# Kernel optimization log

Hardware: AMD Instinct MI355X
Metric: run time of the kernel (lower is better)

The kernel has to match this reference:

```python
import jax, jax.numpy as jnp
import numpy as np

N = 100_000      # num nodes
E = 1_600_000    # num edges
F_IN = 128       # input feature dim
H = 128          # hidden dim
C = 16           # num classes
R = 5            # num relations


def setup_inputs() -> dict:
    key = jax.random.key(0)
    ks = jax.random.split(key, 12)
    x = jax.random.normal(ks[0], (N, F_IN), jnp.float32)
    edge_index = jax.random.randint(ks[1], (2, E), 0, N, dtype=jnp.int64)
    edge_weight = jax.random.uniform(ks[2], (E,), jnp.float32)
    edge_type = jax.random.randint(ks[3], (E,), 0, R, dtype=jnp.int64)
    # RGCNConv params (no basis decomposition): per-relation weight, root, bias
    s1 = 1.0 / np.sqrt(F_IN).astype(np.float32)
    s2 = 1.0 / np.sqrt(H).astype(np.float32)
    W1 = jax.random.normal(ks[4], (R, F_IN, H), jnp.float32) * s1
    root1 = jax.random.normal(ks[5], (F_IN, H), jnp.float32) * s1
    b1 = jnp.zeros((H,), jnp.float32)
    W2 = jax.random.normal(ks[6], (R, H, C), jnp.float32) * s2
    root2 = jax.random.normal(ks[7], (H, C), jnp.float32) * s2
    b2 = jnp.zeros((C,), jnp.float32)
    return {"x": x, "edge_index": edge_index, "edge_weight": edge_weight,
            "edge_type": edge_type, "W1": W1, "root1": root1, "b1": b1,
            "W2": W2, "root2": root2, "b2": b2}


def _rgcn_conv(x, src, dst, ew, et, W, root, b):
    """WeightedRGCNConv: per-relation weighted mean aggregation + relation matmul.

    Equivalent to the torch loop over relations: mask edges of type r,
    propagate with aggr='mean' (PyG RGCNConv default) on messages
    edge_weight * x[src], then h_r @ W[r], summed over r; plus root & bias.
    Vectorized by scattering into (dst, relation) buckets.
    """
    n, r = x.shape[0], W.shape[0]
    m = x[src] * ew[:, None]                       # [E, d_in] messages
    seg = dst * r + et                             # bucket = (dst node, relation)
    sums = jax.ops.segment_sum(m, seg, num_segments=n * r).reshape(n, r, -1)
    cnt = jax.ops.segment_sum(jnp.ones_like(ew), seg, num_segments=n * r)
    cnt = cnt.reshape(n, r, 1)
    agg = sums / jnp.maximum(cnt, 1.0)             # mean; 0 for empty buckets
    out = jnp.einsum('nri,rio->no', agg, W)        # sum_r H_r @ W_r
    return out + x @ root + b


def reference(x, edge_index, edge_weight, edge_type, W1, root1, b1, W2, root2, b2):
    src, dst = edge_index[0], edge_index[1]
    h = _rgcn_conv(x, src, dst, edge_weight, edge_type, W1, root1, b1)
    h = jax.nn.relu(h)  # dropout is identity in eval mode
    out = _rgcn_conv(h, src, dst, edge_weight, edge_type, W2, root2, b2)
    return jax.nn.log_softmax(out, axis=1)
```

## Files before the change

### kernel.cpp

```cpp
#include <hip/hip_runtime.h>

#define N_NODES 100000
#define N_EDGES 1600000
#define N_REL   5
#define M_BUCKETS (N_NODES * N_REL)
#define NCOARSE  196
#define CAP      16384

using bf16x8 = __attribute__((ext_vector_type(8))) short;
using f32x4  = __attribute__((ext_vector_type(4))) float;
using f32x2  = __attribute__((ext_vector_type(2))) float;

__device__ __forceinline__ unsigned short f2bf(float f) {
    unsigned int u = __float_as_uint(f);
    u += 0x7fffu + ((u >> 16) & 1u);
    return (unsigned short)(u >> 16);
}
__device__ __forceinline__ float bflo(unsigned int p) { return __uint_as_float(p << 16); }
__device__ __forceinline__ float bfhi(unsigned int p) { return __uint_as_float(p & 0xffff0000u); }
__device__ __forceinline__ float bfu(unsigned short u) { return __uint_as_float((unsigned int)u << 16); }

__global__ __launch_bounds__(1024) void partition_append(
    const int* __restrict__ src, const int* __restrict__ dstv,
    const float* __restrict__ ew, const int* __restrict__ et,
    int* __restrict__ ccur, int2* __restrict__ pe) {
    __shared__ int lh[256];
    __shared__ int lb[256];
    int tid = threadIdx.x;
    if (tid < 256) lh[tid] = 0;
    __syncthreads();
    int base = blockIdx.x * 4096;
    int key[4], rank[4], meta[4];
    float w[4];
    #pragma unroll
    for (int i = 0; i < 4; ++i) {
        int e = base + i * 1024 + tid;
        key[i] = -1;
        if (e < N_EDGES) {
            int d = dstv[e];
            key[i] = d >> 9;
            meta[i] = src[e] | (et[e] << 17) | ((d & 511) << 20);
            w[i] = ew[e];
            rank[i] = atomicAdd(&lh[key[i]], 1);
        }
    }
    __syncthreads();
    if (tid < 256) {
        int c = lh[tid];
        lb[tid] = c ? atomicAdd(&ccur[tid], c) : 0;
    }
    __syncthreads();
    #pragma unroll
    for (int i = 0; i < 4; ++i)
        if (key[i] >= 0) {
            int pos = lb[key[i]] + rank[i];
            if (pos < CAP)
                pe[((size_t)key[i] << 14) + pos] = make_int2(meta[i], __float_as_int(w[i]));
        }
}

__global__ __launch_bounds__(256) void cscan(const int* __restrict__ ccur,
                                             int* __restrict__ cstart,
                                             int* __restrict__ offs) {
    __shared__ int lds[256];
    int tid = threadIdx.x;
    int v = ccur[tid];
    lds[tid] = v;
    __syncthreads();
    for (int d = 1; d < 256; d <<= 1) {
        int t = (tid >= d) ? lds[tid - d] : 0;
        __syncthreads();
        lds[tid] += t;
        __syncthreads();
    }
    cstart[tid] = lds[tid] - v;
    if (tid == 0) offs[M_BUCKETS] = N_EDGES;
}

__global__ __launch_bounds__(1024) void bucket_sort(
    const int* __restrict__ ccnt, const int* __restrict__ cstart,
    const int2* __restrict__ pe, int2* __restrict__ edges, int* __restrict__ offs) {
    int cb = blockIdx.x;
    int node0 = cb << 9;
    if (node0 >= N_NODES) return;
    int nNodes = N_NODES - node0; if (nNodes > 512) nNodes = 512;
    int nf = nNodes * N_REL;
    __shared__ int hist[2560];
    __shared__ int cur[2560];
    __shared__ int wtot[16];
    __shared__ int woff[16];
    int tid = threadIdx.x;
    int wid = tid >> 6, lane = tid & 63;
    int cnt = ccnt[cb]; if (cnt > CAP) cnt = CAP;
    int gbase = cstart[cb];
    const int2* my = pe + ((size_t)cb << 14);

    for (int i = tid; i < nf; i += 1024) hist[i] = 0;
    __syncthreads();
    for (int i = tid; i < cnt; i += 1024) {
        int m = my[i].x;
        int fb = ((m >> 20) & 511) * N_REL + ((m >> 17) & 7);
        atomicAdd(&hist[fb], 1);
    }
    __syncthreads();

    int t0 = tid * 3;
    int a0 = (t0 + 0 < nf) ? hist[t0 + 0] : 0;
    int a1 = (t0 + 1 < nf) ? hist[t0 + 1] : 0;
    int a2 = (t0 + 2 < nf) ? hist[t0 + 2] : 0;
    int s = a0 + a1 + a2;
    int incl = s;
    #pragma unroll
    for (int d = 1; d < 64; d <<= 1) {
        int t = __shfl_up(incl, d);
        if (lane >= d) incl += t;
    }
    if (lane == 63) wtot[wid] = incl;
    __syncthreads();
    if (wid == 0 && lane < 16) {
        int v = wtot[lane];
        int inc2 = v;
        #pragma unroll
        for (int d = 1; d < 16; d <<= 1) {
            int t = __shfl_up(inc2, d);
            if (lane >= d) inc2 += t;
        }
        woff[lane] = inc2 - v;
    }
    __syncthreads();
    int excl = incl - s + woff[wid];

    int gb0 = node0 * N_REL;
    if (t0 + 0 < nf) { offs[gb0 + t0 + 0] = gbase + excl; cur[t0 + 0] = excl; }
    excl += a0;
    if (t0 + 1 < nf) { offs[gb0 + t0 + 1] = gbase + excl; cur[t0 + 1] = excl; }
    excl += a1;
    if (t0 + 2 < nf) { offs[gb0 + t0 + 2] = gbase + excl; cur[t0 + 2] = excl; }
    __syncthreads();

    for (int i = tid; i < cnt; i += 1024) {
        int2 r = my[i];
        int fb = ((r.x >> 20) & 511) * N_REL + ((r.x >> 17) & 7);
        int pos = gbase + atomicAdd(&cur[fb], 1);
        float wf = __int_as_float(r.y) / (float)hist[fb];
        edges[pos] = make_int2(r.x & 0xFFFFF, __float_as_int(wf));
    }
}

__global__ void cvt_feat(const float* __restrict__ x, ushort* __restrict__ xh,
                         unsigned int* __restrict__ xq) {
    int i = blockIdx.x * blockDim.x + threadIdx.x;
    if (i >= (N_NODES * 128) / 4) return;
    float4 v = reinterpret_cast<const float4*>(x)[i];
    ushort4 o;
    o.x = f2bf(v.x); o.y = f2bf(v.y); o.z = f2bf(v.z); o.w = f2bf(v.w);
    reinterpret_cast<ushort4*>(xh)[i] = o;
    int p = __builtin_amdgcn_cvt_pk_fp8_f32(v.x, v.y, 0, false);
    p = __builtin_amdgcn_cvt_pk_fp8_f32(v.z, v.w, p, true);
    xq[i] = (unsigned int)p;
}

__global__ void cvt_wstack(const float* __restrict__ W, const float* __restrict__ root,
                           ushort* __restrict__ Wt) {
    int t = blockIdx.x * blockDim.x + threadIdx.x;
    int o = blockIdx.y;
    int seg = t >> 7, k = t & 127;
    float v = (seg == 0) ? root[k * 128 + o] : W[(size_t)(seg - 1) * 128 * 128 + k * 128 + o];
    Wt[(size_t)o * 768 + t] = f2bf(v);
}

__global__ void cvt_w2(const float* __restrict__ W2, const float* __restrict__ root2,
                       ushort* __restrict__ Wt2s) {
    int i = blockIdx.x * blockDim.x + threadIdx.x;
    if (i >= 96 * 128) return;
    int o = i >> 7, k = i & 127;
    float v = (o < 16) ? root2[k * 16 + o]
                       : W2[((size_t)((o >> 4) - 1) * 128 + k) * 16 + (o & 15)];
    Wt2s[i] = f2bf(v);
}

__global__ __launch_bounds__(256) void gather_all(
    const ushort* __restrict__ featq,
    const int2* __restrict__ edges,
    const int* __restrict__ offs,
    ushort* __restrict__ A,
    int node0) {
    int n = __builtin_amdgcn_readfirstlane(node0 + blockIdx.x * 4 + (threadIdx.x >> 6));
    int lane = threadIdx.x & 63;
    int b0 = n * N_REL;
    int o0 = __builtin_amdgcn_readfirstlane(offs[b0 + 0]);
    int o1 = __builtin_amdgcn_readfirstlane(offs[b0 + 1]);
    int o2 = __builtin_amdgcn_readfirstlane(offs[b0 + 2]);
    int o3 = __builtin_amdgcn_readfirstlane(offs[b0 + 3]);
    int o4 = __builtin_amdgcn_readfirstlane(offs[b0 + 4]);
    int o5 = __builtin_amdgcn_readfirstlane(offs[b0 + 5]);
    unsigned int* Ap = reinterpret_cast<unsigned int*>(A) + (size_t)(n - node0) * 320;

    int deg = o5 - o0;
    if (deg <= 64) {
        int2 er = (o0 + lane < o5) ? edges[o0 + lane] : make_int2(0, 0);
        unsigned long long bp =
              (unsigned long long)(unsigned)(o1 - o0)
            | ((unsigned long long)(unsigned)(o2 - o0) << 8)
            | ((unsigned long long)(unsigned)(o3 - o0) << 16)
            | ((unsigned long long)(unsigned)(o4 - o0) << 24)
            | ((unsigned long long)(unsigned)deg << 32);
        float ax = 0.f, ay = 0.f;
        int seg = 0;
        auto flushAt = [&](int jj) {
            while (seg < 5 && jj == (int)((bp >> (seg * 8)) & 0xFFull)) {
                Ap[64 * seg + lane] =
                    (unsigned int)f2bf(ax) | ((unsigned int)f2bf(ay) << 16);
                ax = 0.f; ay = 0.f; ++seg;
            }
        };
        int deg8 = (deg + 7) & ~7;
        for (int j = 0; j < deg8; j += 8) {
            unsigned short q[8];
            float w[8];
            #pragma unroll
            for (int u = 0; u < 8; ++u) {
                int m = __builtin_amdgcn_readlane(er.x, j + u);
                q[u] = featq[((size_t)(m & 0x1FFFF) << 6) + lane];
            }
            #pragma unroll
            for (int u = 0; u < 8; ++u)
                w[u] = __uint_as_float(__builtin_amdgcn_readlane(er.y, j + u));
            #pragma unroll
            for (int u = 0; u < 8; ++u) {
                flushAt(j + u);
                f32x2 f = __builtin_amdgcn_cvt_pk_f32_fp8((int)q[u], false);
                ax = fmaf(w[u], f.x, ax); ay = fmaf(w[u], f.y, ay);
            }
        }
        while (seg < 5) {
            Ap[64 * seg + lane] =
                (unsigned int)f2bf(ax) | ((unsigned int)f2bf(ay) << 16);
            ax = 0.f; ay = 0.f; ++seg;
        }
    } else {
        int o[6] = {o0, o1, o2, o3, o4, o5};
        #pragma unroll
        for (int r = 0; r < 5; ++r) {
            int s0 = o[r], e1 = o[r + 1];
            float ax = 0.f, ay = 0.f;
            for (int base = s0; base < e1; base += 64) {
                int idx = base + lane;
                int2 er = (idx < e1) ? edges[idx] : make_int2(0, 0);
                int m = e1 - base; if (m > 64) m = 64;
                for (int j = 0; j < m; ++j) {
                    int mm = __builtin_amdgcn_readlane(er.x, j);
                    float w = __uint_as_float(__builtin_amdgcn_readlane(er.y, j));
                    unsigned short q = featq[((size_t)(mm & 0x1FFFF) << 6) + lane];
                    f32x2 f = __builtin_amdgcn_cvt_pk_f32_fp8((int)q, false);
                    ax = fmaf(w, f.x, ax);
                    ay = fmaf(w, f.y, ay);
                }
            }
            Ap[64 * r + lane] = (unsigned int)f2bf(ax) | ((unsigned int)f2bf(ay) << 16);
        }
    }
}

__global__ __launch_bounds__(256) void gemmL1(
    const ushort* __restrict__ xh,
    const ushort* __restrict__ A,
    const ushort* __restrict__ Wt,
    const float* __restrict__ bias,
    ushort* __restrict__ h,
    int row0, int nrows) {
    __shared__ ushort As[128 * 64];
    __shared__ ushort Bs[128 * 64];
    const int tid = threadIdx.x, lane = tid & 63, wave = tid >> 6;
    const int m0 = blockIdx.x * 128;

    constexpr int MF = 4, NF = 4;
    const int wr0 = (wave >> 1) * 64;
    const int wc0 = (wave & 1) * 64;

    f32x4 acc[MF][NF] = {};

    for (int ks = 0; ks < 12; ++ks) {
        #pragma unroll
        for (int u = 0; u < 4; ++u) {
            int idx = tid + u * 256;
            int row = idx >> 3, slot = idx & 7;
            float4 v;
            if (ks < 2) {
                int gr = row0 + m0 + row; if (gr >= N_NODES) gr = N_NODES - 1;
                v = *reinterpret_cast<const float4*>(xh + (size_t)gr * 128 + ks * 64 + slot * 8);
            } else {
                v = *reinterpret_cast<const float4*>(
                    A + (size_t)(m0 + row) * 640 + (ks - 2) * 64 + slot * 8);
            }
            int byte = row * 128 + ((slot ^ (row & 7)) << 4);
            *reinterpret_cast<float4*>(reinterpret_cast<char*>(As) + byte) = v;
        }
        #pragma unroll
        for (int u = 0; u < 4; ++u) {
            int idx = tid + u * 256;
            int row = idx >> 3, slot = idx & 7;
            float4 v = *reinterpret_cast<const float4*>(
                Wt + (size_t)row * 768 + ks * 64 + slot * 8);
            int byte = row * 128 + ((slot ^ (row & 7)) << 4);
            *reinterpret_cast<float4*>(reinterpret_cast<char*>(Bs) + byte) = v;
        }
        __syncthreads();

        #pragma unroll
        for (int kh = 0; kh < 2; ++kh) {
            bf16x8 af[MF], bfr[NF];
            #pragma unroll
            for (int m = 0; m < MF; ++m) {
                int row = wr0 + m * 16 + (lane & 15);
                int slot = kh * 4 + (lane >> 4);
                int byte = row * 128 + ((slot ^ (row & 7)) << 4);
                af[m] = *reinterpret_cast<const bf16x8*>(
                    reinterpret_cast<const char*>(As) + byte);
            }
            #pragma unroll
            for (int nn = 0; nn < NF; ++nn) {
                int row = wc0 + nn * 16 + (lane & 15);
                int slot = kh * 4 + (lane >> 4);
                int byte = row * 128 + ((slot ^ (row & 7)) << 4);
                bfr[nn] = *reinterpret_cast<const bf16x8*>(
                    reinterpret_cast<const char*>(Bs) + byte);
            }
            #pragma unroll
            for (int m = 0; m < MF; ++m)
                #pragma unroll
                for (int nn = 0; nn < NF; ++nn)
                    acc[m][nn] = __builtin_amdgcn_mfma_f32_16x16x32_bf16(
                        af[m], bfr[nn], acc[m][nn], 0, 0, 0);
        }
        __syncthreads();
    }

    #pragma unroll
    for (int m = 0; m < MF; ++m) {
        int rloc = wr0 + m * 16 + (lane >> 4) * 4;
        #pragma unroll
        for (int nn = 0; nn < NF; ++nn) {
            int c = wc0 + nn * 16 + (lane & 15);
            float bv = bias[c];
            #pragma unroll
            for (int q = 0; q < 4; ++q) {
                int lrow = m0 + rloc + q;
                if (lrow < nrows) {
                    int grow = row0 + lrow;
                    float v = fmaxf(acc[m][nn][q] + bv, 0.f);
                    h[(size_t)grow * 128 + c] = f2bf(v);
                }
            }
        }
    }
}

__global__ __launch_bounds__(256) void gemm96(
    const ushort* __restrict__ h, const ushort* __restrict__ Wt,
    ushort* __restrict__ Yh) {
    __shared__ ushort As[128 * 128];
    __shared__ ushort Bs[96 * 128];
    const int tid = threadIdx.x, lane = tid & 63, wave = tid >> 6;
    const int m0 = blockIdx.x * 128;

    #pragma unroll
    for (int u = 0; u < 8; ++u) {
        int idx = tid + u * 256;
        int row = idx >> 4, slot = idx & 15;
        int gr = m0 + row; if (gr >= N_NODES) gr = N_NODES - 1;
        float4 v = *reinterpret_cast<const float4*>(h + (size_t)gr * 128 + slot * 8);
        int byte = row * 256 + ((slot ^ (row & 15)) << 4);
        *reinterpret_cast<float4*>(reinterpret_cast<char*>(As) + byte) = v;
    }
    #pragma unroll
    for (int u = 0; u < 6; ++u) {
        int idx = tid + u * 256;
        int row = idx >> 4, slot = idx & 15;
        float4 v = *reinterpret_cast<const float4*>(Wt + (size_t)row * 128 + slot * 8);
        int byte = row * 256 + ((slot ^ (row & 15)) << 4);
        *reinterpret_cast<float4*>(reinterpret_cast<char*>(Bs) + byte) = v;
    }
    __syncthreads();

    f32x4 acc[2][6] = {};
    #pragma unroll
    for (int ks = 0; ks < 4; ++ks) {
        bf16x8 af[2], bfr[6];
        #pragma unroll
        for (int m = 0; m < 2; ++m) {
            int row = wave * 32 + m * 16 + (lane & 15);
            int slot = ks * 4 + (lane >> 4);
            int byte = row * 256 + ((slot ^ (row & 15)) << 4);
            af[m] = *reinterpret_cast<const bf16x8*>(reinterpret_cast<const char*>(As) + byte);
        }
        #pragma unroll
        for (int nn = 0; nn < 6; ++nn) {
            int row = nn * 16 + (lane & 15);
            int slot = ks * 4 + (lane >> 4);
            int byte = row * 256 + ((slot ^ (row & 15)) << 4);
            bfr[nn] = *reinterpret_cast<const bf16x8*>(reinterpret_cast<const char*>(Bs) + byte);
        }
        #pragma unroll
        for (int m = 0; m < 2; ++m)
            #pragma unroll
            for (int nn = 0; nn < 6; ++nn)
                acc[m][nn] = __builtin_amdgcn_mfma_f32_16x16x32_bf16(
                    af[m], bfr[nn], acc[m][nn], 0, 0, 0);
    }

    #pragma unroll
    for (int m = 0; m < 2; ++m) {
        int rloc = m0 + wave * 32 + m * 16 + (lane >> 4) * 4;
        #pragma unroll
        for (int nn = 0; nn < 6; ++nn) {
            int c = nn * 16 + (lane & 15);
            #pragma unroll
            for (int q = 0; q < 4; ++q) {
                int row = rloc + q;
                if (row < N_NODES) Yh[(size_t)row * 96 + c] = f2bf(acc[m][nn][q]);
            }
        }
    }
}

__global__ __launch_bounds__(256) void agg2_softmax(
    const ushort* __restrict__ Yh, const int2* __restrict__ edges,
    const int* __restrict__ offs, const float* __restrict__ b2,
    float* __restrict__ out) {
    int wave = threadIdx.x >> 6, lane = threadIdx.x & 63;
    int q = lane >> 4, c = lane & 15;
    int n = (blockIdx.x * 4 + wave) * 4 + q;
    int nn = (n < N_NODES) ? n : N_NODES - 1;
    int o0 = offs[nn * N_REL], o5 = offs[nn * N_REL + 5];
    int deg = o5 - o0;

    float val = bfu(Yh[(size_t)nn * 96 + c]) + b2[c];

    for (int b = 0; b < deg; b += 16) {
        int idx = o0 + b + c;
        int2 er = (idx < o5) ? edges[idx] : make_int2(0, 0);
        #pragma unroll
        for (int j = 0; j < 16; ++j) {
            int m = __shfl(er.x, q * 16 + j);
            float w = __uint_as_float(__shfl(er.y, q * 16 + j));
            int s = m & 0x1FFFF;
            int rel = (m >> 17) & 7;
            val = fmaf(w, bfu(Yh[(size_t)s * 96 + 16 + rel * 16 + c]), val);
        }
    }

    float mx = val;
    #pragma unroll
    for (int i = 1; i < 16; i <<= 1) mx = fmaxf(mx, __shfl_xor(mx, i));
    float ex = expf(val - mx);
    float ssum = ex;
    #pragma unroll
    for (int i = 1; i < 16; i <<= 1) ssum += __shfl_xor(ssum, i);
    float r = val - mx - logf(ssum);
    if (n < N_NODES) out[(size_t)n * 16 + c] = r;
}

extern "C" void kernel_launch(void* const* d_in, const int* in_sizes, int n_in,
                              void* d_out, int out_size, void* d_ws, size_t ws_size,
                              hipStream_t stream) {
    const float* x     = (const float*)d_in[0];
    const int*   ei    = (const int*)d_in[1];
    const int*   src   = ei;
    const int*   dst   = ei + N_EDGES;
    const float* ew    = (const float*)d_in[2];
    const int*   et    = (const int*)d_in[3];
    const float* W1    = (const float*)d_in[4];
    const float* root1 = (const float*)d_in[5];
    const float* b1    = (const float*)d_in[6];
    const float* W2    = (const float*)d_in[7];
    const float* root2 = (const float*)d_in[8];
    const float* b2    = (const float*)d_in[9];
    float* out = (float*)d_out;

    char* ws = (char*)d_ws;
    int*    offs    = (int*)ws;
    int*    ccur    = (int*)(ws + 2000896);
    int*    cstart  = (int*)(ws + 2001920);
    int2*   edges   = (int2*)(ws + 2004096);
    ushort* xh      = (ushort*)(ws + 14804096);
    ushort* h       = (ushort*)(ws + 40404096);
    ushort* Wt1     = (ushort*)(ws + 66004096);
    ushort* Wt2s    = (ushort*)(ws + 66200704);
    unsigned int* xq = (unsigned int*)(ws + 66225280);
    int2*   pe      = (int2*)(ws + 79026176);
    ushort* Abuf    = (ushort*)(ws + 79026176);
    ushort* Yh      = (ushort*)(ws + 79026176);

    const int chunk = (ws_size >= 220000000ull) ? N_NODES : 25000;
    const int nch   = N_NODES / chunk;

    cvt_feat<<<((N_NODES * 128 / 4) + 255) / 256, 256, 0, stream>>>(x, xh, xq);
    cvt_wstack<<<dim3(3, 128), 256, 0, stream>>>(W1, root1, Wt1);
    cvt_w2<<<(96 * 128 + 255) / 256, 256, 0, stream>>>(W2, root2, Wt2s);

    hipMemsetAsync(ccur, 0, 1024, stream);
    partition_append<<<(N_EDGES + 4095) / 4096, 1024, 0, stream>>>(src, dst, ew, et, ccur, pe);
    cscan<<<1, 256, 0, stream>>>(ccur, cstart, offs);
    bucket_sort<<<NCOARSE, 1024, 0, stream>>>(ccur, cstart, pe, edges, offs);

    for (int cc = 0; cc < nch; ++cc) {
        gather_all<<<chunk / 4, 256, 0, stream>>>(
            (const ushort*)xq, edges, offs, Abuf, cc * chunk);
        gemmL1<<<(chunk + 127) / 128, 256, 0, stream>>>(
            xh, Abuf, Wt1, b1, h, cc * chunk, chunk);
    }

    gemm96<<<(N_NODES + 127) / 128, 256, 0, stream>>>(h, Wt2s, Yh);
    agg2_softmax<<<(N_NODES + 15) / 16, 256, 0, stream>>>(Yh, edges, offs, b2, out);
}
```

Baseline: 217.1 us.

## Pad relation buckets to even length and gather two edges per wave step

Each (node, relation) bucket in the sorted edge list is padded to an even length with zero-weight dummy edges, and per-node offsets are repacked into a base plus packed relation boundaries (nbase/nbp). The per-bucket offsets array goes away. In the gather kernel, each half-wave processes a different edge and loads 4 fp8 features per lane as a 32-bit word, then the halves are combined with a cross-half shuffle. This doubles the memory-level parallelism per gather step and widens loads, at the cost of padding edges, extra shuffles and a larger edge buffer with slack.

```diff
diff --git a/kernel.cpp b/kernel.cpp
--- a/kernel.cpp
+++ b/kernel.cpp
@@ -3,9 +3,9 @@
 #define N_NODES 100000
 #define N_EDGES 1600000
 #define N_REL   5
-#define M_BUCKETS (N_NODES * N_REL)
 #define NCOARSE  196
 #define CAP      16384
+#define SLACK    2560
 
 using bf16x8 = __attribute__((ext_vector_type(8))) short;
 using f32x4  = __attribute__((ext_vector_type(4))) float;
@@ -16,8 +16,6 @@
     u += 0x7fffu + ((u >> 16) & 1u);
     return (unsigned short)(u >> 16);
 }
-__device__ __forceinline__ float bflo(unsigned int p) { return __uint_as_float(p << 16); }
-__device__ __forceinline__ float bfhi(unsigned int p) { return __uint_as_float(p & 0xffff0000u); }
 __device__ __forceinline__ float bfu(unsigned short u) { return __uint_as_float((unsigned int)u << 16); }
 
 __global__ __launch_bounds__(1024) void partition_append(
@@ -60,11 +58,10 @@
 }
 
 __global__ __launch_bounds__(256) void cscan(const int* __restrict__ ccur,
-                                             int* __restrict__ cstart,
-                                             int* __restrict__ offs) {
+                                             int* __restrict__ cstart) {
     __shared__ int lds[256];
     int tid = threadIdx.x;
-    int v = ccur[tid];
+    int v = ccur[tid] + SLACK;
     lds[tid] = v;
     __syncthreads();
     for (int d = 1; d < 256; d <<= 1) {
@@ -74,12 +71,12 @@
         __syncthreads();
     }
     cstart[tid] = lds[tid] - v;
-    if (tid == 0) offs[M_BUCKETS] = N_EDGES;
 }
 
 __global__ __launch_bounds__(1024) void bucket_sort(
     const int* __restrict__ ccnt, const int* __restrict__ cstart,
-    const int2* __restrict__ pe, int2* __restrict__ edges, int* __restrict__ offs) {
+    const int2* __restrict__ pe, int2* __restrict__ edges,
+    int* __restrict__ nbase, int2* __restrict__ nbp) {
     int cb = blockIdx.x;
     int node0 = cb << 9;
     if (node0 >= N_NODES) return;
@@ -99,15 +96,14 @@
     __syncthreads();
     for (int i = tid; i < cnt; i += 1024) {
         int m = my[i].x;
-        int fb = ((m >> 20) & 511) * N_REL + ((m >> 17) & 7);
-        atomicAdd(&hist[fb], 1);
+        atomicAdd(&hist[((m >> 20) & 511) * N_REL + ((m >> 17) & 7)], 1);
     }
     __syncthreads();
 
     int t0 = tid * 3;
-    int a0 = (t0 + 0 < nf) ? hist[t0 + 0] : 0;
-    int a1 = (t0 + 1 < nf) ? hist[t0 + 1] : 0;
-    int a2 = (t0 + 2 < nf) ? hist[t0 + 2] : 0;
+    int a0 = (t0 + 0 < nf) ? ((hist[t0 + 0] + 1) & ~1) : 0;
+    int a1 = (t0 + 1 < nf) ? ((hist[t0 + 1] + 1) & ~1) : 0;
+    int a2 = (t0 + 2 < nf) ? ((hist[t0 + 2] + 1) & ~1) : 0;
     int s = a0 + a1 + a2;
     int incl = s;
     #pragma unroll
@@ -129,13 +125,25 @@
     }
     __syncthreads();
     int excl = incl - s + woff[wid];
-
-    int gb0 = node0 * N_REL;
-    if (t0 + 0 < nf) { offs[gb0 + t0 + 0] = gbase + excl; cur[t0 + 0] = excl; }
+    if (t0 + 0 < nf) cur[t0 + 0] = excl;
     excl += a0;
-    if (t0 + 1 < nf) { offs[gb0 + t0 + 1] = gbase + excl; cur[t0 + 1] = excl; }
+    if (t0 + 1 < nf) cur[t0 + 1] = excl;
     excl += a1;
-    if (t0 + 2 < nf) { offs[gb0 + t0 + 2] = gbase + excl; cur[t0 + 2] = excl; }
+    if (t0 + 2 < nf) cur[t0 + 2] = excl;
+    __syncthreads();
+
+    for (int i = tid; i < nf; i += 1024)
+        if (hist[i] & 1)
+            edges[(size_t)gbase + cur[i] + hist[i]] = make_int2(0, 0);
+    for (int i = tid; i < nNodes; i += 1024) {
+        int b = i * N_REL;
+        int c0 = cur[b];
+        int B1 = cur[b + 1] - c0, B2 = cur[b + 2] - c0;
+        int B3 = cur[b + 3] - c0, B4 = cur[b + 4] - c0;
+        int degp = cur[b + 4] + ((hist[b + 4] + 1) & ~1) - c0;
+        nbase[node0 + i] = gbase + c0;
+        nbp[node0 + i] = make_int2(B1 | (B2 << 8) | (B3 << 16) | (B4 << 24), degp);
+    }
     __syncthreads();
 
     for (int i = tid; i < cnt; i += 1024) {
@@ -180,84 +188,96 @@
 }
 
 __global__ __launch_bounds__(256) void gather_all(
-    const ushort* __restrict__ featq,
+    const unsigned int* __restrict__ xq,
     const int2* __restrict__ edges,
-    const int* __restrict__ offs,
+    const int* __restrict__ nbase,
+    const int2* __restrict__ nbp,
     ushort* __restrict__ A,
     int node0) {
     int n = __builtin_amdgcn_readfirstlane(node0 + blockIdx.x * 4 + (threadIdx.x >> 6));
     int lane = threadIdx.x & 63;
-    int b0 = n * N_REL;
-    int o0 = __builtin_amdgcn_readfirstlane(offs[b0 + 0]);
-    int o1 = __builtin_amdgcn_readfirstlane(offs[b0 + 1]);
-    int o2 = __builtin_amdgcn_readfirstlane(offs[b0 + 2]);
-    int o3 = __builtin_amdgcn_readfirstlane(offs[b0 + 3]);
-    int o4 = __builtin_amdgcn_readfirstlane(offs[b0 + 4]);
-    int o5 = __builtin_amdgcn_readfirstlane(offs[b0 + 5]);
-    unsigned int* Ap = reinterpret_cast<unsigned int*>(A) + (size_t)(n - node0) * 320;
-
-    int deg = o5 - o0;
-    if (deg <= 64) {
-        int2 er = (o0 + lane < o5) ? edges[o0 + lane] : make_int2(0, 0);
-        unsigned long long bp =
-              (unsigned long long)(unsigned)(o1 - o0)
-            | ((unsigned long long)(unsigned)(o2 - o0) << 8)
-            | ((unsigned long long)(unsigned)(o3 - o0) << 16)
-            | ((unsigned long long)(unsigned)(o4 - o0) << 24)
-            | ((unsigned long long)(unsigned)deg << 32);
-        float ax = 0.f, ay = 0.f;
+    int half = lane >> 5, lane31 = lane & 31;
+    int o0   = __builtin_amdgcn_readfirstlane(nbase[n]);
+    int bx   = __builtin_amdgcn_readfirstlane(nbp[n].x);
+    int degp = __builtin_amdgcn_readfirstlane(nbp[n].y);
+    uint2* Ap2 = reinterpret_cast<uint2*>(A + (size_t)(n - node0) * 640);
+
+    if (degp <= 64) {
+        int2 er = (lane < degp) ? edges[o0 + lane] : make_int2(0, 0);
+        unsigned long long bp = (unsigned long long)(unsigned)bx
+                              | ((unsigned long long)(unsigned)degp << 32);
+        float a0 = 0.f, a1 = 0.f, a2 = 0.f, a3 = 0.f;
         int seg = 0;
         auto flushAt = [&](int jj) {
             while (seg < 5 && jj == (int)((bp >> (seg * 8)) & 0xFFull)) {
-                Ap[64 * seg + lane] =
-                    (unsigned int)f2bf(ax) | ((unsigned int)f2bf(ay) << 16);
-                ax = 0.f; ay = 0.f; ++seg;
+                float t0 = a0 + __shfl_xor(a0, 32);
+                float t1 = a1 + __shfl_xor(a1, 32);
+                float t2 = a2 + __shfl_xor(a2, 32);
+                float t3 = a3 + __shfl_xor(a3, 32);
+                if (lane < 32) {
+                    uint2 v;
+                    v.x = (unsigned int)f2bf(t0) | ((unsigned int)f2bf(t1) << 16);
+                    v.y = (unsigned int)f2bf(t2) | ((unsigned int)f2bf(t3) << 16);
+                    Ap2[seg * 32 + lane31] = v;
+                }
+                a0 = a1 = a2 = a3 = 0.f; ++seg;
             }
         };
-        int deg8 = (deg + 7) & ~7;
+        int deg8 = (degp + 7) & ~7;
         for (int j = 0; j < deg8; j += 8) {
-            unsigned short q[8];
-            float w[8];
-            #pragma unroll
-            for (int u = 0; u < 8; ++u) {
-                int m = __builtin_amdgcn_readlane(er.x, j + u);
-                q[u] = featq[((size_t)(m & 0x1FFFF) << 6) + lane];
-            }
-            #pragma unroll
-            for (int u = 0; u < 8; ++u)
-                w[u] = __uint_as_float(__builtin_amdgcn_readlane(er.y, j + u));
-            #pragma unroll
-            for (int u = 0; u < 8; ++u) {
-                flushAt(j + u);
-                f32x2 f = __builtin_amdgcn_cvt_pk_f32_fp8((int)q[u], false);
-                ax = fmaf(w[u], f.x, ax); ay = fmaf(w[u], f.y, ay);
+            unsigned int q[4]; float wv[4];
+            #pragma unroll
+            for (int s2 = 0; s2 < 4; ++s2) {
+                int jv = j + 2 * s2 + half;
+                int m = __shfl(er.x, jv);
+                wv[s2] = __uint_as_float(__shfl(er.y, jv));
+                q[s2] = xq[((size_t)(m & 0x1FFFF) << 5) + lane31];
+            }
+            #pragma unroll
+            for (int s2 = 0; s2 < 4; ++s2) {
+                flushAt(j + 2 * s2);
+                f32x2 flo = __builtin_amdgcn_cvt_pk_f32_fp8((int)q[s2], false);
+                f32x2 fhi = __builtin_amdgcn_cvt_pk_f32_fp8((int)q[s2], true);
+                a0 = fmaf(wv[s2], flo.x, a0); a1 = fmaf(wv[s2], flo.y, a1);
+                a2 = fmaf(wv[s2], fhi.x, a2); a3 = fmaf(wv[s2], fhi.y, a3);
             }
         }
         while (seg < 5) {
-            Ap[64 * seg + lane] =
-                (unsigned int)f2bf(ax) | ((unsigned int)f2bf(ay) << 16);
-            ax = 0.f; ay = 0.f; ++seg;
+            float t0 = a0 + __shfl_xor(a0, 32);
+            float t1 = a1 + __shfl_xor(a1, 32);
+            float t2 = a2 + __shfl_xor(a2, 32);
+            float t3 = a3 + __shfl_xor(a3, 32);
+            if (lane < 32) {
+                uint2 v;
+                v.x = (unsigned int)f2bf(t0) | ((unsigned int)f2bf(t1) << 16);
+                v.y = (unsigned int)f2bf(t2) | ((unsigned int)f2bf(t3) << 16);
+                Ap2[seg * 32 + lane31] = v;
+            }
+            a0 = a1 = a2 = a3 = 0.f; ++seg;
         }
     } else {
-        int o[6] = {o0, o1, o2, o3, o4, o5};
+        const ushort* fq = reinterpret_cast<const ushort*>(xq);
+        int B[6];
+        B[0] = 0; B[1] = bx & 0xFF; B[2] = (bx >> 8) & 0xFF;
+        B[3] = (bx >> 16) & 0xFF; B[4] = (unsigned)bx >> 24; B[5] = degp;
+        unsigned int* Ap = reinterpret_cast<unsigned int*>(Ap2);
         #pragma unroll
         for (int r = 0; r < 5; ++r) {
-            int s0 = o[r], e1 = o[r + 1];
+            int s0 = o0 + B[r], e1 = o0 + B[r + 1];
             float ax = 0.f, ay = 0.f;
             for (int base = s0; base < e1; base += 64) {
-                int idx = base + lane;
-                int2 er = (idx < e1) ? edges[idx] : make_int2(0, 0);
+                int2 er = (base + lane < e1) ? edges[base + lane] : make_int2(0, 0);
                 int m = e1 - base; if (m > 64) m = 64;
                 for (int j = 0; j < m; ++j) {
                     int mm = __builtin_amdgcn_readlane(er.x, j);
                     float w = __uint_as_float(__builtin_amdgcn_readlane(er.y, j));
-                    unsigned short q = featq[((size_t)(mm & 0x1FFFF) << 6) + lane];
-                    f32x2 f = __builtin_amdgcn_cvt_pk_f32_fp8((int)q, false);
+                    ushort qv = fq[((size_t)(mm & 0x1FFFF) << 6) + lane];
+                    f32x2 f = __builtin_amdgcn_cvt_pk_f32_fp8((int)qv, false);
                     ax = fmaf(w, f.x, ax);
                     ay = fmaf(w, f.y, ay);
                 }
             }
-            Ap[64 * r + lane] = (unsigned int)f2bf(ax) | ((unsigned int)f2bf(ay) << 16);
+            Ap[r * 64 + lane] = (unsigned int)f2bf(ax) | ((unsigned int)f2bf(ay) << 16);
         }
     }
 }
@@ -426,20 +446,19 @@
 
 __global__ __launch_bounds__(256) void agg2_softmax(
     const ushort* __restrict__ Yh, const int2* __restrict__ edges,
-    const int* __restrict__ offs, const float* __restrict__ b2,
-    float* __restrict__ out) {
+    const int* __restrict__ nbase, const int2* __restrict__ nbp,
+    const float* __restrict__ b2, float* __restrict__ out) {
     int wave = threadIdx.x >> 6, lane = threadIdx.x & 63;
     int q = lane >> 4, c = lane & 15;
     int n = (blockIdx.x * 4 + wave) * 4 + q;
     int nn = (n < N_NODES) ? n : N_NODES - 1;
-    int o0 = offs[nn * N_REL], o5 = offs[nn * N_REL + 5];
-    int deg = o5 - o0;
+    int o0 = nbase[nn];
+    int degp = nbp[nn].y;
 
     float val = bfu(Yh[(size_t)nn * 96 + c]) + b2[c];
 
-    for (int b = 0; b < deg; b += 16) {
-        int idx = o0 + b + c;
-        int2 er = (idx < o5) ? edges[idx] : make_int2(0, 0);
+    for (int b = 0; b < degp; b += 16) {
+        int2 er = (b + c < degp) ? edges[o0 + b + c] : make_int2(0, 0);
         #pragma unroll
         for (int j = 0; j < 16; ++j) {
             int m = __shfl(er.x, q * 16 + j);
@@ -479,18 +498,19 @@
     float* out = (float*)d_out;
 
     char* ws = (char*)d_ws;
-    int*    offs    = (int*)ws;
-    int*    ccur    = (int*)(ws + 2000896);
-    int*    cstart  = (int*)(ws + 2001920);
-    int2*   edges   = (int2*)(ws + 2004096);
-    ushort* xh      = (ushort*)(ws + 14804096);
-    ushort* h       = (ushort*)(ws + 40404096);
-    ushort* Wt1     = (ushort*)(ws + 66004096);
-    ushort* Wt2s    = (ushort*)(ws + 66200704);
-    unsigned int* xq = (unsigned int*)(ws + 66225280);
-    int2*   pe      = (int2*)(ws + 79026176);
-    ushort* Abuf    = (ushort*)(ws + 79026176);
-    ushort* Yh      = (ushort*)(ws + 79026176);
+    int*    ccur    = (int*)ws;
+    int*    cstart  = (int*)(ws + 1024);
+    int*    nbase   = (int*)(ws + 4096);
+    int2*   nbp     = (int2*)(ws + 404096);
+    int2*   edges   = (int2*)(ws + 1204096);
+    ushort* xh      = (ushort*)(ws + 18018304);
+    ushort* h       = (ushort*)(ws + 43618304);
+    ushort* Wt1     = (ushort*)(ws + 69218304);
+    ushort* Wt2s    = (ushort*)(ws + 69414912);
+    unsigned int* xq = (unsigned int*)(ws + 69439488);
+    int2*   pe      = (int2*)(ws + 82239488);
+    ushort* Abuf    = (ushort*)(ws + 82239488);
+    ushort* Yh      = (ushort*)(ws + 82239488);
 
     const int chunk = (ws_size >= 220000000ull) ? N_NODES : 25000;
     const int nch   = N_NODES / chunk;
@@ -501,16 +521,16 @@
 
     hipMemsetAsync(ccur, 0, 1024, stream);
     partition_append<<<(N_EDGES + 4095) / 4096, 1024, 0, stream>>>(src, dst, ew, et, ccur, pe);
-    cscan<<<1, 256, 0, stream>>>(ccur, cstart, offs);
-    bucket_sort<<<NCOARSE, 1024, 0, stream>>>(ccur, cstart, pe, edges, offs);
+    cscan<<<1, 256, 0, stream>>>(ccur, cstart);
+    bucket_sort<<<NCOARSE, 1024, 0, stream>>>(ccur, cstart, pe, edges, nbase, nbp);
 
     for (int cc = 0; cc < nch; ++cc) {
         gather_all<<<chunk / 4, 256, 0, stream>>>(
-            (const ushort*)xq, edges, offs, Abuf, cc * chunk);
+            xq, edges, nbase, nbp, Abuf, cc * chunk);
         gemmL1<<<(chunk + 127) / 128, 256, 0, stream>>>(
             xh, Abuf, Wt1, b1, h, cc * chunk, chunk);
     }
 
     gemm96<<<(N_NODES + 127) / 128, 256, 0, stream>>>(h, Wt2s, Yh);
-    agg2_softmax<<<(N_NODES + 15) / 16, 256, 0, stream>>>(Yh, edges, offs, b2, out);
-}
+    agg2_softmax<<<(N_NODES + 15) / 16, 256, 0, stream>>>(Yh, edges, nbase, nbp, b2, out);
+}
```

Measured after the change: 215.5 us. About the same (-0.7%).

## Fuse layer-2 projection GEMM into layer-1 GEMM and compact per-node bucket offsets

Applied to the files above, without the earlier changes.

The layer-2 projection (h @ [root2|W2]) now runs inside the layer-1 GEMM kernel. The ReLU'd hidden tile is written to LDS instead of global memory, and the 96-column GEMM reads it from there. This removes the separate gemm96 launch and the round trip of the hidden activations through HBM. Per-(node,relation) offsets are replaced by a per-node base plus packed relation boundaries and degree, which cuts offset reads in the gather and aggregation kernels. The fused kernel loads Wt2 fragments straight from global memory rather than staging them in LDS, and the packing assumes each relation prefix fits in 8 bits.

```diff
diff --git a/kernel.cpp b/kernel.cpp
--- a/kernel.cpp
+++ b/kernel.cpp
@@ -3,7 +3,6 @@
 #define N_NODES 100000
 #define N_EDGES 1600000
 #define N_REL   5
-#define M_BUCKETS (N_NODES * N_REL)
 #define NCOARSE  196
 #define CAP      16384
 
@@ -16,8 +15,6 @@
     u += 0x7fffu + ((u >> 16) & 1u);
     return (unsigned short)(u >> 16);
 }
-__device__ __forceinline__ float bflo(unsigned int p) { return __uint_as_float(p << 16); }
-__device__ __forceinline__ float bfhi(unsigned int p) { return __uint_as_float(p & 0xffff0000u); }
 __device__ __forceinline__ float bfu(unsigned short u) { return __uint_as_float((unsigned int)u << 16); }
 
 __global__ __launch_bounds__(1024) void partition_append(
@@ -60,8 +57,7 @@
 }
 
 __global__ __launch_bounds__(256) void cscan(const int* __restrict__ ccur,
-                                             int* __restrict__ cstart,
-                                             int* __restrict__ offs) {
+                                             int* __restrict__ cstart) {
     __shared__ int lds[256];
     int tid = threadIdx.x;
     int v = ccur[tid];
@@ -74,12 +70,12 @@
         __syncthreads();
     }
     cstart[tid] = lds[tid] - v;
-    if (tid == 0) offs[M_BUCKETS] = N_EDGES;
 }
 
 __global__ __launch_bounds__(1024) void bucket_sort(
     const int* __restrict__ ccnt, const int* __restrict__ cstart,
-    const int2* __restrict__ pe, int2* __restrict__ edges, int* __restrict__ offs) {
+    const int2* __restrict__ pe, int2* __restrict__ edges,
+    int* __restrict__ nbase, int2* __restrict__ nbp) {
     int cb = blockIdx.x;
     int node0 = cb << 9;
     if (node0 >= N_NODES) return;
@@ -99,8 +95,7 @@
     __syncthreads();
     for (int i = tid; i < cnt; i += 1024) {
         int m = my[i].x;
-        int fb = ((m >> 20) & 511) * N_REL + ((m >> 17) & 7);
-        atomicAdd(&hist[fb], 1);
+        atomicAdd(&hist[((m >> 20) & 511) * N_REL + ((m >> 17) & 7)], 1);
     }
     __syncthreads();
 
@@ -129,13 +124,22 @@
     }
     __syncthreads();
     int excl = incl - s + woff[wid];
-
-    int gb0 = node0 * N_REL;
-    if (t0 + 0 < nf) { offs[gb0 + t0 + 0] = gbase + excl; cur[t0 + 0] = excl; }
+    if (t0 + 0 < nf) cur[t0 + 0] = excl;
     excl += a0;
-    if (t0 + 1 < nf) { offs[gb0 + t0 + 1] = gbase + excl; cur[t0 + 1] = excl; }
+    if (t0 + 1 < nf) cur[t0 + 1] = excl;
     excl += a1;
-    if (t0 + 2 < nf) { offs[gb0 + t0 + 2] = gbase + excl; cur[t0 + 2] = excl; }
+    if (t0 + 2 < nf) cur[t0 + 2] = excl;
+    __syncthreads();
+
+    for (int i = tid; i < nNodes; i += 1024) {
+        int b = i * N_REL;
+        int c0 = cur[b];
+        int B1 = cur[b + 1] - c0, B2 = cur[b + 2] - c0;
+        int B3 = cur[b + 3] - c0, B4 = cur[b + 4] - c0;
+        int deg = cur[b + 4] + hist[b + 4] - c0;
+        nbase[node0 + i] = gbase + c0;
+        nbp[node0 + i] = make_int2(B1 | (B2 << 8) | (B3 << 16) | (B4 << 24), deg);
+    }
     __syncthreads();
 
     for (int i = tid; i < cnt; i += 1024) {
@@ -182,29 +186,21 @@
 __global__ __launch_bounds__(256) void gather_all(
     const ushort* __restrict__ featq,
     const int2* __restrict__ edges,
-    const int* __restrict__ offs,
+    const int* __restrict__ nbase,
+    const int2* __restrict__ nbp,
     ushort* __restrict__ A,
     int node0) {
     int n = __builtin_amdgcn_readfirstlane(node0 + blockIdx.x * 4 + (threadIdx.x >> 6));
     int lane = threadIdx.x & 63;
-    int b0 = n * N_REL;
-    int o0 = __builtin_amdgcn_readfirstlane(offs[b0 + 0]);
-    int o1 = __builtin_amdgcn_readfirstlane(offs[b0 + 1]);
-    int o2 = __builtin_amdgcn_readfirstlane(offs[b0 + 2]);
-    int o3 = __builtin_amdgcn_readfirstlane(offs[b0 + 3]);
-    int o4 = __builtin_amdgcn_readfirstlane(offs[b0 + 4]);
-    int o5 = __builtin_amdgcn_readfirstlane(offs[b0 + 5]);
+    int o0  = __builtin_amdgcn_readfirstlane(nbase[n]);
+    int bx  = __builtin_amdgcn_readfirstlane(nbp[n].x);
+    int deg = __builtin_amdgcn_readfirstlane(nbp[n].y);
     unsigned int* Ap = reinterpret_cast<unsigned int*>(A) + (size_t)(n - node0) * 320;
 
-    int deg = o5 - o0;
     if (deg <= 64) {
-        int2 er = (o0 + lane < o5) ? edges[o0 + lane] : make_int2(0, 0);
-        unsigned long long bp =
-              (unsigned long long)(unsigned)(o1 - o0)
-            | ((unsigned long long)(unsigned)(o2 - o0) << 8)
-            | ((unsigned long long)(unsigned)(o3 - o0) << 16)
-            | ((unsigned long long)(unsigned)(o4 - o0) << 24)
-            | ((unsigned long long)(unsigned)deg << 32);
+        int2 er = (lane < deg) ? edges[o0 + lane] : make_int2(0, 0);
+        unsigned long long bp = (unsigned long long)(unsigned)bx
+                              | ((unsigned long long)(unsigned)deg << 32);
         float ax = 0.f, ay = 0.f;
         int seg = 0;
         auto flushAt = [&](int jj) {
@@ -239,38 +235,41 @@
             ax = 0.f; ay = 0.f; ++seg;
         }
     } else {
-        int o[6] = {o0, o1, o2, o3, o4, o5};
+        int B[6];
+        B[0] = 0; B[1] = bx & 0xFF; B[2] = (bx >> 8) & 0xFF;
+        B[3] = (bx >> 16) & 0xFF; B[4] = (unsigned)bx >> 24; B[5] = deg;
         #pragma unroll
         for (int r = 0; r < 5; ++r) {
-            int s0 = o[r], e1 = o[r + 1];
+            int s0 = o0 + B[r], e1 = o0 + B[r + 1];
             float ax = 0.f, ay = 0.f;
             for (int base = s0; base < e1; base += 64) {
-                int idx = base + lane;
-                int2 er = (idx < e1) ? edges[idx] : make_int2(0, 0);
+                int2 er = (base + lane < e1) ? edges[base + lane] : make_int2(0, 0);
                 int m = e1 - base; if (m > 64) m = 64;
                 for (int j = 0; j < m; ++j) {
                     int mm = __builtin_amdgcn_readlane(er.x, j);
                     float w = __uint_as_float(__builtin_amdgcn_readlane(er.y, j));
-                    unsigned short q = featq[((size_t)(mm & 0x1FFFF) << 6) + lane];
-                    f32x2 f = __builtin_amdgcn_cvt_pk_f32_fp8((int)q, false);
+                    unsigned short qv = featq[((size_t)(mm & 0x1FFFF) << 6) + lane];
+                    f32x2 f = __builtin_amdgcn_cvt_pk_f32_fp8((int)qv, false);
                     ax = fmaf(w, f.x, ax);
                     ay = fmaf(w, f.y, ay);
                 }
             }
-            Ap[64 * r + lane] = (unsigned int)f2bf(ax) | ((unsigned int)f2bf(ay) << 16);
-        }
-    }
-}
-
-__global__ __launch_bounds__(256) void gemmL1(
+            Ap[r * 64 + lane] = (unsigned int)f2bf(ax) | ((unsigned int)f2bf(ay) << 16);
+        }
+    }
+}
+
+__global__ __launch_bounds__(256) void gemmL1f(
     const ushort* __restrict__ xh,
     const ushort* __restrict__ A,
     const ushort* __restrict__ Wt,
     const float* __restrict__ bias,
-    ushort* __restrict__ h,
+    const ushort* __restrict__ Wt2,
+    ushort* __restrict__ Yh,
     int row0, int nrows) {
-    __shared__ ushort As[128 * 64];
-    __shared__ ushort Bs[128 * 64];
+    __shared__ ushort lds[128 * 128];
+    ushort* As = lds;
+    ushort* Bs = lds + 128 * 64;
     const int tid = threadIdx.x, lane = tid & 63, wave = tid >> 6;
     const int m0 = blockIdx.x * 128;
 
@@ -345,45 +344,16 @@
             float bv = bias[c];
             #pragma unroll
             for (int q = 0; q < 4; ++q) {
-                int lrow = m0 + rloc + q;
-                if (lrow < nrows) {
-                    int grow = row0 + lrow;
-                    float v = fmaxf(acc[m][nn][q] + bv, 0.f);
-                    h[(size_t)grow * 128 + c] = f2bf(v);
-                }
-            }
-        }
-    }
-}
-
-__global__ __launch_bounds__(256) void gemm96(
-    const ushort* __restrict__ h, const ushort* __restrict__ Wt,
-    ushort* __restrict__ Yh) {
-    __shared__ ushort As[128 * 128];
-    __shared__ ushort Bs[96 * 128];
-    const int tid = threadIdx.x, lane = tid & 63, wave = tid >> 6;
-    const int m0 = blockIdx.x * 128;
-
-    #pragma unroll
-    for (int u = 0; u < 8; ++u) {
-        int idx = tid + u * 256;
-        int row = idx >> 4, slot = idx & 15;
-        int gr = m0 + row; if (gr >= N_NODES) gr = N_NODES - 1;
-        float4 v = *reinterpret_cast<const float4*>(h + (size_t)gr * 128 + slot * 8);
-        int byte = row * 256 + ((slot ^ (row & 15)) << 4);
-        *reinterpret_cast<float4*>(reinterpret_cast<char*>(As) + byte) = v;
-    }
-    #pragma unroll
-    for (int u = 0; u < 6; ++u) {
-        int idx = tid + u * 256;
-        int row = idx >> 4, slot = idx & 15;
-        float4 v = *reinterpret_cast<const float4*>(Wt + (size_t)row * 128 + slot * 8);
-        int byte = row * 256 + ((slot ^ (row & 15)) << 4);
-        *reinterpret_cast<float4*>(reinterpret_cast<char*>(Bs) + byte) = v;
-    }
-    __syncthreads();
-
-    f32x4 acc[2][6] = {};
+                int row = rloc + q;
+                float v = fmaxf(acc[m][nn][q] + bv, 0.f);
+                int byte = row * 256 + ((((c >> 3) ^ (row & 15)) << 4)) + (c & 7) * 2;
+                *reinterpret_cast<ushort*>(reinterpret_cast<char*>(lds) + byte) = f2bf(v);
+            }
+        }
+    }
+    __syncthreads();
+
+    f32x4 acc2[2][6] = {};
     #pragma unroll
     for (int ks = 0; ks < 4; ++ks) {
         bf16x8 af[2], bfr[6];
@@ -392,33 +362,36 @@
             int row = wave * 32 + m * 16 + (lane & 15);
             int slot = ks * 4 + (lane >> 4);
             int byte = row * 256 + ((slot ^ (row & 15)) << 4);
-            af[m] = *reinterpret_cast<const bf16x8*>(reinterpret_cast<const char*>(As) + byte);
+            af[m] = *reinterpret_cast<const bf16x8*>(
+                reinterpret_cast<const char*>(lds) + byte);
         }
         #pragma unroll
         for (int nn = 0; nn < 6; ++nn) {
             int row = nn * 16 + (lane & 15);
             int slot = ks * 4 + (lane >> 4);
-            int byte = row * 256 + ((slot ^ (row & 15)) << 4);
-            bfr[nn] = *reinterpret_cast<const bf16x8*>(reinterpret_cast<const char*>(Bs) + byte);
+            bfr[nn] = *reinterpret_cast<const bf16x8*>(
+                Wt2 + (size_t)row * 128 + slot * 8);
         }
         #pragma unroll
         for (int m = 0; m < 2; ++m)
             #pragma unroll
             for (int nn = 0; nn < 6; ++nn)
-                acc[m][nn] = __builtin_amdgcn_mfma_f32_16x16x32_bf16(
-                    af[m], bfr[nn], acc[m][nn], 0, 0, 0);
+                acc2[m][nn] = __builtin_amdgcn_mfma_f32_16x16x32_bf16(
+                    af[m], bfr[nn], acc2[m][nn], 0, 0, 0);
     }
 
     #pragma unroll
     for (int m = 0; m < 2; ++m) {
-        int rloc = m0 + wave * 32 + m * 16 + (lane >> 4) * 4;
+        int rloc = wave * 32 + m * 16 + (lane >> 4) * 4;
         #pragma unroll
         for (int nn = 0; nn < 6; ++nn) {
             int c = nn * 16 + (lane & 15);
             #pragma unroll
             for (int q = 0; q < 4; ++q) {
-                int row = rloc + q;
-                if (row < N_NODES) Yh[(size_t)row * 96 + c] = f2bf(acc[m][nn][q]);
+                int lrow = m0 + rloc + q;
+                int grow = row0 + lrow;
+                if (lrow < nrows && grow < N_NODES)
+                    Yh[(size_t)grow * 96 + c] = f2bf(acc2[m][nn][q]);
             }
         }
     }
@@ -426,20 +399,19 @@
 
 __global__ __launch_bounds__(256) void agg2_softmax(
     const ushort* __restrict__ Yh, const int2* __restrict__ edges,
-    const int* __restrict__ offs, const float* __restrict__ b2,
-    float* __restrict__ out) {
+    const int* __restrict__ nbase, const int2* __restrict__ nbp,
+    const float* __restrict__ b2, float* __restrict__ out) {
     int wave = threadIdx.x >> 6, lane = threadIdx.x & 63;
     int q = lane >> 4, c = lane & 15;
     int n = (blockIdx.x * 4 + wave) * 4 + q;
     int nn = (n < N_NODES) ? n : N_NODES - 1;
-    int o0 = offs[nn * N_REL], o5 = offs[nn * N_REL + 5];
-    int deg = o5 - o0;
+    int o0 = nbase[nn];
+    int deg = nbp[nn].y;
 
     float val = bfu(Yh[(size_t)nn * 96 + c]) + b2[c];
 
     for (int b = 0; b < deg; b += 16) {
-        int idx = o0 + b + c;
-        int2 er = (idx < o5) ? edges[idx] : make_int2(0, 0);
+        int2 er = (b + c < deg) ? edges[o0 + b + c] : make_int2(0, 0);
         #pragma unroll
         for (int j = 0; j < 16; ++j) {
             int m = __shfl(er.x, q * 16 + j);
@@ -479,21 +451,22 @@
     float* out = (float*)d_out;
 
     char* ws = (char*)d_ws;
-    int*    offs    = (int*)ws;
-    int*    ccur    = (int*)(ws + 2000896);
-    int*    cstart  = (int*)(ws + 2001920);
-    int2*   edges   = (int2*)(ws + 2004096);
-    ushort* xh      = (ushort*)(ws + 14804096);
-    ushort* h       = (ushort*)(ws + 40404096);
-    ushort* Wt1     = (ushort*)(ws + 66004096);
-    ushort* Wt2s    = (ushort*)(ws + 66200704);
-    unsigned int* xq = (unsigned int*)(ws + 66225280);
-    int2*   pe      = (int2*)(ws + 79026176);
-    ushort* Abuf    = (ushort*)(ws + 79026176);
-    ushort* Yh      = (ushort*)(ws + 79026176);
-
-    const int chunk = (ws_size >= 220000000ull) ? N_NODES : 25000;
+    int*    ccur    = (int*)ws;
+    int*    cstart  = (int*)(ws + 1024);
+    int*    nbase   = (int*)(ws + 4096);
+    int2*   nbp     = (int2*)(ws + 404096);
+    int2*   edges   = (int2*)(ws + 1204096);
+    ushort* xh      = (ushort*)(ws + 18018304);
+    ushort* Wt1     = (ushort*)(ws + 43618304);
+    ushort* Wt2s    = (ushort*)(ws + 43814912);
+    unsigned int* xq = (unsigned int*)(ws + 43839488);
+    int2*   pe      = (int2*)(ws + 56639488);
+    ushort* Abuf    = (ushort*)(ws + 56639488);
+
+    const int chunk = (ws_size >= 225000000ull) ? N_NODES : 25000;
     const int nch   = N_NODES / chunk;
+    ushort* Yh = (ushort*)(ws + 56639488 +
+        (chunk == N_NODES ? 128122880ull : 32112640ull));
 
     cvt_feat<<<((N_NODES * 128 / 4) + 255) / 256, 256, 0, stream>>>(x, xh, xq);
     cvt_wstack<<<dim3(3, 128), 256, 0, stream>>>(W1, root1, Wt1);
@@ -501,16 +474,16 @@
 
     hipMemsetAsync(ccur, 0, 1024, stream);
     partition_append<<<(N_EDGES + 4095) / 4096, 1024, 0, stream>>>(src, dst, ew, et, ccur, pe);
-    cscan<<<1, 256, 0, stream>>>(ccur, cstart, offs);
-    bucket_sort<<<NCOARSE, 1024, 0, stream>>>(ccur, cstart, pe, edges, offs);
+    cscan<<<1, 256, 0, stream>>>(ccur, cstart);
+    bucket_sort<<<NCOARSE, 1024, 0, stream>>>(ccur, cstart, pe, edges, nbase, nbp);
 
     for (int cc = 0; cc < nch; ++cc) {
         gather_all<<<chunk / 4, 256, 0, stream>>>(
-            (const ushort*)xq, edges, offs, Abuf, cc * chunk);
-        gemmL1<<<(chunk + 127) / 128, 256, 0, stream>>>(
-            xh, Abuf, Wt1, b1, h, cc * chunk, chunk);
-    }
-
-    gemm96<<<(N_NODES + 127) / 128, 256, 0, stream>>>(h, Wt2s, Yh);
-    agg2_softmax<<<(N_NODES + 15) / 16, 256, 0, stream>>>(Yh, edges, offs, b2, out);
-}
+            (const ushort*)xq, edges, nbase, nbp, Abuf, cc * chunk);
+        gemmL1f<<<(chunk + 127) / 128, 256, 0, stream>>>(
+            xh, Abuf, Wt1, b1, Wt2s, Yh, cc * chunk, chunk);
+    }
+
+    agg2_softmax<<<(N_NODES + 15) / 16, 256, 0, stream>>>(
+        Yh, edges, nbase, nbp, b2, out);
+}
```

New measurement: 210.1 us. 3.2% less time.
